# Optimization experiments

Measured on AMD Instinct MI355X. Metric: run time of the kernel, lower is better.

Reference implementation:

```python
import jax, jax.numpy as jnp
import numpy as np

D = 384
MAXPOS = 6

def setup_inputs() -> dict:
    key = jax.random.key(0)
    ks = jax.random.split(key, 20)
    B, Lt, Lh, E = 4, 1024, 512, 64
    inp = {
        'text': jax.random.normal(ks[0], (B, Lt, D), jnp.float32),
        'html': jax.random.normal(ks[1], (B, Lh, D), jnp.float32),
        'H2Hmask': jax.random.randint(ks[2], (B, Lh, Lh), 0, E, jnp.int32),
        'T2Tmask': (jax.random.uniform(ks[3], (B, Lt, Lt)) < 0.1).astype(jnp.float32),
        'H2Tmask': (jax.random.uniform(ks[4], (B, Lh, Lt)) < 0.1).astype(jnp.float32),
        'T2Hmask': (jax.random.uniform(ks[5], (B, Lt, Lh)) < 0.1).astype(jnp.float32),
        'positionembedding': jax.random.normal(ks[6], (2 * MAXPOS + 1, D), jnp.float32) * 0.02,
        'htmledgeembedding': jax.random.normal(ks[7], (E, D), jnp.float32) * 0.02,
    }
    names = ['W_V_T', 'W_V_H', 'W_Q_H2H', 'W_K_H2H', 'W_Q_H2T', 'W_K_H2T',
             'W_Q_T2H', 'W_K_T2H', 'W_Q_T2T', 'W_K_T2T']
    lim = np.sqrt(6.0 / (D + D))  # glorot_uniform
    for i, n in enumerate(names):
        inp[n] = jax.random.uniform(ks[8 + i], (D, D), jnp.float32, -lim, lim)
    return inp


def _forward(text, html, H2Hmask, T2Tmask, H2Tmask, T2Hmask,
             positionembedding, htmledgeembedding,
             W_V_T, W_V_H, W_Q_H2H, W_K_H2H, W_Q_H2T, W_K_H2T,
             W_Q_T2H, W_K_T2H, W_Q_T2T, W_K_T2T):
    B, Lt, _ = text.shape
    Lh = html.shape[1]
    scale = 1.0 / jnp.sqrt(jnp.float32(D))

    text_v = text @ W_V_T   # (B,Lt,D)
    html_v = html @ W_V_H   # (B,Lh,D)

    # ---- H2H: content + gathered edge-embedding bias ----
    # sum_d q[b,i,d] * (k[b,j,d] + edge[H2Hmask[b,i,j], d])
    #   = (q k^T)[b,i,j] + (q E^T)[b,i, H2Hmask[b,i,j]]
    h2h_q = html @ W_Q_H2H
    h2h_k = html @ W_K_H2H
    h2h_content = jnp.einsum('bid,bjd->bij', h2h_q, h2h_k)
    qe = h2h_q @ htmledgeembedding.T                       # (B,Lh,E)
    h2h_bias = jnp.take_along_axis(qe, H2Hmask, axis=-1)   # (B,Lh,Lh)
    h2h_e = (h2h_content + h2h_bias) * scale
    h2h_e = h2h_e - 10000.0 * (H2Hmask == 0).astype(jnp.float32)
    html1 = jax.nn.softmax(h2h_e, axis=-1) @ html_v

    # ---- H2T ----
    h2t_e = jnp.einsum('bid,bjd->bij', html @ W_Q_H2T, text @ W_K_H2T) * scale
    h2t_e = h2t_e - 10000.0 * H2Tmask
    html2 = jax.nn.softmax(h2t_e, axis=-1) @ text_v

    # ---- T2H (note: original code never applies T2Hmask) ----
    t2h_e = jnp.einsum('bid,bjd->bij', text @ W_Q_T2H, html @ W_K_T2H) * scale
    text1 = jax.nn.softmax(t2h_e, axis=-1) @ html_v

    # ---- T2T: content + relative-position bias ----
    idx = jnp.arange(Lt, dtype=jnp.int32)
    pos_ids = jnp.clip(idx[None, :] - idx[:, None], -MAXPOS, MAXPOS) + MAXPOS  # (Lt,Lt)
    t2t_q = text @ W_Q_T2T
    t2t_k = text @ W_K_T2T
    t2t_content = jnp.einsum('bid,bjd->bij', t2t_q, t2t_k)
    qp = t2t_q @ positionembedding.T                       # (B,Lt,2*MAXPOS+1)
    t2t_bias = jnp.take_along_axis(
        qp, jnp.broadcast_to(pos_ids[None], (B, Lt, Lt)), axis=-1)
    t2t_e = (t2t_content + t2t_bias) * scale
    t2t_e = t2t_e - 10000.0 * T2Tmask
    text2 = jax.nn.softmax(t2t_e, axis=-1) @ text_v

    # concat updated text (Lt) and html (Lh) along seq axis -> (B, Lt+Lh, D)
    return jnp.concatenate([text1 + text2, html1 + html2], axis=1)


def reference(text, html, H2Hmask, T2Tmask, H2Tmask, T2Hmask,
              positionembedding, htmledgeembedding,
              W_V_T, W_V_H, W_Q_H2H, W_K_H2H, W_Q_H2T, W_K_H2T,
              W_Q_T2H, W_K_T2H, W_Q_T2T, W_K_T2T):
    return _forward(text, html, H2Hmask, T2Tmask, H2Tmask, T2Hmask,
                    positionembedding, htmledgeembedding,
                    W_V_T, W_V_H, W_Q_H2H, W_K_H2H, W_Q_H2T, W_K_H2T,
                    W_Q_T2H, W_K_T2H, W_Q_T2T, W_K_T2T)
```

## Files before the change

### kernel.cpp

```cpp
#include <hip/hip_runtime.h>
#include <math.h>

typedef unsigned short u16;
typedef unsigned int u32;
typedef __attribute__((ext_vector_type(8))) short short8;
typedef __attribute__((ext_vector_type(4))) float f32x4;

__device__ __forceinline__ u16 f2bf(float f) {
    u32 u = __float_as_uint(f);
    u = (u + 0x7FFFu + ((u >> 16) & 1u)) >> 16;
    return (u16)u;
}
__device__ __forceinline__ float bf2f(u16 h) {
    return __uint_as_float(((u32)h) << 16);
}


__global__ __launch_bounds__(256)
void cvt4(const float4* __restrict__ a, int na4,
          const float4* __restrict__ b, int nb4,
          const float4* __restrict__ c, int nc4,
          const float4* __restrict__ d, int nd4,
          u16* __restrict__ oa, u16* __restrict__ ob,
          u16* __restrict__ oc, u16* __restrict__ od)
{
    int idx = blockIdx.x * 256 + threadIdx.x;
    const int tot = na4 + nb4 + nc4 + nd4;
    for (; idx < tot; idx += gridDim.x * 256) {
        float4 v; u16* o;
        int t = idx;
        if (t < na4)      { v = a[t]; o = oa + (long)t * 4; }
        else if ((t -= na4) < nb4) { v = b[t]; o = ob + (long)t * 4; }
        else if ((t -= nb4) < nc4) { v = c[t]; o = oc + (long)t * 4; }
        else { t -= nc4;    v = d[t]; o = od + (long)t * 4; }
        u32 lo = (u32)f2bf(v.x) | ((u32)f2bf(v.y) << 16);
        u32 hi = (u32)f2bf(v.z) | ((u32)f2bf(v.w) << 16);
        uint2 pk; pk.x = lo; pk.y = hi;
        *reinterpret_cast<uint2*>(o) = pk;
    }
}

struct WP { const float* p[10]; };
struct WD { u16* d[10]; };

__global__ __launch_bounds__(1024)
void wtrans(WP w, WD wd)
{
    __shared__ float t[32][33];
    const int z = blockIdx.z;
    const float* W = w.p[z];
    const int k = blockIdx.x * 32 + threadIdx.y;
    const int n = blockIdx.y * 32 + threadIdx.x;
    t[threadIdx.y][threadIdx.x] = W[k * 384 + n];
    __syncthreads();
    const int no = blockIdx.y * 32 + threadIdx.y;
    const int ko = blockIdx.x * 32 + threadIdx.x;
    wd.d[z][no * 384 + ko] = f2bf(t[threadIdx.x][threadIdx.y]);
}

__device__ __forceinline__ void mfma_core128(
    const u16* __restrict__ A, int lda,
    const u16* __restrict__ B, int ldb, int K,
    u16* __restrict__ As, u16* __restrict__ Bs,
    f32x4 (&acc)[4][4])
{
    const int tid  = threadIdx.x;
    const int wid  = tid >> 6;
    const int lane = tid & 63;
    const int wr = wid >> 1, wc = wid & 1;
    const int lane15 = lane & 15;
    const int kg = (lane >> 4) * 8;
    const int srow = lane >> 2;
    const int scol = (lane & 3) * 8;

    #pragma unroll
    for (int i = 0; i < 4; ++i)
        #pragma unroll
        for (int j = 0; j < 4; ++j)
            acc[i][j] = (f32x4){0.f, 0.f, 0.f, 0.f};

    for (int k0 = 0; k0 < K; k0 += 32) {
        #pragma unroll
        for (int i = 0; i < 2; ++i) {
            const int rg = (wid * 2 + i) * 16;
            const u16* ga = A + (long)(rg + srow) * lda + (k0 + scol);
            const u16* gb = B + (long)(rg + srow) * ldb + (k0 + scol);
            u16* la = As + (wid * 2 + i) * 512;
            u16* lb = Bs + (wid * 2 + i) * 512;
            __builtin_amdgcn_global_load_lds(
                (const __attribute__((address_space(1))) void*)ga,
                (__attribute__((address_space(3))) void*)la, 16, 0, 0);
            __builtin_amdgcn_global_load_lds(
                (const __attribute__((address_space(1))) void*)gb,
                (__attribute__((address_space(3))) void*)lb, 16, 0, 0);
        }
        __syncthreads();

        short8 af[4], bf[4];
        #pragma unroll
        for (int mi = 0; mi < 4; ++mi)
            af[mi] = *reinterpret_cast<const short8*>(
                As + (wr * 64 + mi * 16 + lane15) * 32 + kg);
        #pragma unroll
        for (int ni = 0; ni < 4; ++ni)
            bf[ni] = *reinterpret_cast<const short8*>(
                Bs + (wc * 64 + ni * 16 + lane15) * 32 + kg);
        #pragma unroll
        for (int mi = 0; mi < 4; ++mi)
            #pragma unroll
            for (int ni = 0; ni < 4; ++ni)
                acc[mi][ni] = __builtin_amdgcn_mfma_f32_16x16x32_bf16(
                    af[mi], bf[ni], acc[mi][ni], 0, 0, 0);
        __syncthreads();
    }
}

struct Seg {
    const u16* A; const u16* B; float* C;
    long sA, sB, sC;
    int lda, ldb, ldc, K, nbx, nbxSh, start, pad;
};
struct Segs { Seg s[6]; };

template<int NSEG>
__global__ __launch_bounds__(256)
void gemm_grouped(Segs d)
{
    __shared__ __align__(16) u16 As[4096];
    __shared__ __align__(16) u16 Bs[4096];
    const int bid = blockIdx.x;
    Seg sg = d.s[0];
    if (NSEG > 1 && bid >= d.s[1].start) sg = d.s[1];
    if (NSEG > 2 && bid >= d.s[2].start) sg = d.s[2];
    if (NSEG > 3 && bid >= d.s[3].start) sg = d.s[3];
    if (NSEG > 4 && bid >= d.s[4].start) sg = d.s[4];
    if (NSEG > 5 && bid >= d.s[5].start) sg = d.s[5];

    const int local = bid - sg.start;
    const int bx = local & (sg.nbx - 1);
    const int by = local >> sg.nbxSh;
    const int z  = blockIdx.y;
    const int m0 = bx * 128, n0 = by * 128;

    const u16* A = sg.A + (long)z * sg.sA + (long)m0 * sg.lda;
    const u16* B = sg.B + (long)z * sg.sB + (long)n0 * sg.ldb;

    f32x4 acc[4][4];
    mfma_core128(A, sg.lda, B, sg.ldb, sg.K, As, Bs, acc);

    const int tid = threadIdx.x;
    const int wid = tid >> 6, lane = tid & 63;
    const int wr = wid >> 1, wc = wid & 1;
    const int lane15 = lane & 15;
    const int r0 = (lane >> 4) * 4;

    float* C = sg.C + (long)z * sg.sC;
    #pragma unroll
    for (int mi = 0; mi < 4; ++mi)
        #pragma unroll
        for (int r = 0; r < 4; ++r) {
            const int row = m0 + wr * 64 + mi * 16 + r0 + r;
            float* crow = C + (long)row * sg.ldc + n0 + wc * 64 + lane15;
            #pragma unroll
            for (int ni = 0; ni < 4; ++ni)
                crow[ni * 16] = acc[mi][ni][r];
        }
}

struct PSeg {
    const u16* A; const u16* Bw; u16* QK; u16* VT;
    int lvtSh, vtOff, nbx, nbxSh, start, pad;
};
struct PSegs { PSeg s[2]; };

__global__ __launch_bounds__(256)
void proj_grouped(PSegs d)
{
    __shared__ __align__(16) u16 As[4096];
    __shared__ __align__(16) u16 Bs[4096];
    const int bid = blockIdx.x;
    PSeg sg = d.s[0];
    if (bid >= d.s[1].start) sg = d.s[1];

    const int local = bid - sg.start;
    const int bx = local & (sg.nbx - 1);
    const int by = local >> sg.nbxSh;
    const int m0 = bx * 128, n0 = by * 128;

    const u16* A = sg.A + (long)m0 * 384;
    const u16* B = sg.Bw + (long)n0 * 384;

    f32x4 acc[4][4];
    mfma_core128(A, 384, B, 384, 384, As, Bs, acc);

    const int tid = threadIdx.x;
    const int wid = tid >> 6, lane = tid & 63;
    const int wr = wid >> 1, wc = wid & 1;
    const int lane15 = lane & 15;
    const int r0 = (lane >> 4) * 4;
    const int lmask = (1 << sg.lvtSh) - 1;

    if (n0 < 384) {
        #pragma unroll
        for (int mi = 0; mi < 4; ++mi) {
            const int row = m0 + wr * 64 + mi * 16 + r0;
            const int bz = row >> sg.lvtSh;
            const int l  = row & lmask;
            #pragma unroll
            for (int ni = 0; ni < 4; ++ni) {
                const int col = n0 + wc * 64 + ni * 16 + lane15;
                u32 lo = (u32)f2bf(acc[mi][ni][0]) | ((u32)f2bf(acc[mi][ni][1]) << 16);
                u32 hi = (u32)f2bf(acc[mi][ni][2]) | ((u32)f2bf(acc[mi][ni][3]) << 16);
                uint2 pk; pk.x = lo; pk.y = hi;
                *reinterpret_cast<uint2*>(
                    sg.VT + ((long)bz * 384 + col) * 1536 + sg.vtOff + l) = pk;
            }
        }
    } else {
        #pragma unroll
        for (int mi = 0; mi < 4; ++mi)
            #pragma unroll
            for (int r = 0; r < 4; ++r) {
                const int row = m0 + wr * 64 + mi * 16 + r0 + r;
                u16* qrow = sg.QK + (long)row * 1536 + (n0 - 384) + wc * 64 + lane15;
                #pragma unroll
                for (int ni = 0; ni < 4; ++ni)
                    qrow[ni * 16] = f2bf(acc[mi][ni][r]);
            }
    }
}


__device__ __forceinline__ float blockReduceMax(float v, float* red, int tid) {
    #pragma unroll
    for (int o = 32; o >= 1; o >>= 1) v = fmaxf(v, __shfl_xor(v, o));
    if ((tid & 63) == 0) red[tid >> 6] = v;
    __syncthreads();
    return fmaxf(fmaxf(red[0], red[1]), fmaxf(red[2], red[3]));
}
__device__ __forceinline__ float blockReduceSum(float v, float* red, int tid) {
    #pragma unroll
    for (int o = 32; o >= 1; o >>= 1) v += __shfl_xor(v, o);
    if ((tid & 63) == 0) red[4 + (tid >> 6)] = v;
    __syncthreads();
    return red[4] + red[5] + red[6] + red[7];
}

__global__ __launch_bounds__(256)
void softmax_fused(const float* __restrict__ scoresH, u16* __restrict__ probsH,
                   const float* __restrict__ scoresT, u16* __restrict__ probsT,
                   const float* __restrict__ qe, const float* __restrict__ qp,
                   const int* __restrict__ H2Hmask,
                   const float* __restrict__ H2Tmask,
                   const float* __restrict__ T2Tmask, float scale)
{
    const int bid = blockIdx.x;
    const int tid = threadIdx.x;
    __shared__ float qsh[64];
    __shared__ float red[8];

    if (bid < 2048) {
        const int b = bid >> 9, i = bid & 511;
        const long rbase = ((long)b * 512 + i) * 1536;
        const float* rowS = scoresH + rbase;
        u16* rowP = probsH + rbase;
        const int*   mrow  = H2Hmask + ((long)b * 512 + i) * 512;
        const float* m2row = H2Tmask + ((long)b * 512 + i) * 1024;
        if (tid < 64) qsh[tid] = qe[((long)b * 512 + i) * 128 + tid];
        __syncthreads();

        float x[2]; float mx = -1e30f;
        #pragma unroll
        for (int t = 0; t < 2; ++t) {
            const int j = tid + t * 256;
            const int m = mrow[j];
            float v = (rowS[j] + qsh[m]) * scale - 10000.f * (m == 0 ? 1.f : 0.f);
            x[t] = v; mx = fmaxf(mx, v);
        }
        mx = blockReduceMax(mx, red, tid);
        float s = 0.f;
        #pragma unroll
        for (int t = 0; t < 2; ++t) { x[t] = __expf(x[t] - mx); s += x[t]; }
        s = blockReduceSum(s, red, tid);
        float inv = 1.f / s;
        #pragma unroll
        for (int t = 0; t < 2; ++t) rowP[tid + t * 256] = f2bf(x[t] * inv);

        float y[4]; mx = -1e30f;
        #pragma unroll
        for (int t = 0; t < 4; ++t) {
            const int jj = tid + t * 256;
            float v = rowS[512 + jj] * scale - 10000.f * m2row[jj];
            y[t] = v; mx = fmaxf(mx, v);
        }
        mx = blockReduceMax(mx, red, tid);
        s = 0.f;
        #pragma unroll
        for (int t = 0; t < 4; ++t) { y[t] = __expf(y[t] - mx); s += y[t]; }
        s = blockReduceSum(s, red, tid);
        inv = 1.f / s;
        #pragma unroll
        for (int t = 0; t < 4; ++t) rowP[512 + tid + t * 256] = f2bf(y[t] * inv);
    } else {
        const int bid2 = bid - 2048;
        const int b = bid2 >> 10, i = bid2 & 1023;
        const long rbase = ((long)b * 1024 + i) * 1536;
        const float* rowS = scoresT + rbase;
        u16* rowP = probsT + rbase;
        const float* m2row = T2Tmask + ((long)b * 1024 + i) * 1024;
        if (tid < 13) qsh[tid] = qp[((long)b * 1024 + i) * 128 + tid];
        __syncthreads();

        float x[2]; float mx = -1e30f;
        #pragma unroll
        for (int t = 0; t < 2; ++t) {
            const int j = tid + t * 256;
            float v = rowS[j] * scale;
            x[t] = v; mx = fmaxf(mx, v);
        }
        mx = blockReduceMax(mx, red, tid);
        float s = 0.f;
        #pragma unroll
        for (int t = 0; t < 2; ++t) { x[t] = __expf(x[t] - mx); s += x[t]; }
        s = blockReduceSum(s, red, tid);
        float inv = 1.f / s;
        #pragma unroll
        for (int t = 0; t < 2; ++t) rowP[tid + t * 256] = f2bf(x[t] * inv);

        float y[4]; mx = -1e30f;
        #pragma unroll
        for (int t = 0; t < 4; ++t) {
            const int jj = tid + t * 256;
            int pos = jj - i;
            pos = (pos < -6 ? -6 : (pos > 6 ? 6 : pos)) + 6;
            float v = (rowS[512 + jj] + qsh[pos]) * scale - 10000.f * m2row[jj];
            y[t] = v; mx = fmaxf(mx, v);
        }
        mx = blockReduceMax(mx, red, tid);
        s = 0.f;
        #pragma unroll
        for (int t = 0; t < 4; ++t) { y[t] = __expf(y[t] - mx); s += y[t]; }
        s = blockReduceSum(s, red, tid);
        inv = 1.f / s;
        #pragma unroll
        for (int t = 0; t < 4; ++t) rowP[512 + tid + t * 256] = f2bf(y[t] * inv);
    }
}


extern "C" void kernel_launch(void* const* d_in, const int* in_sizes, int n_in,
                              void* d_out, int out_size, void* d_ws, size_t ws_size,
                              hipStream_t stream)
{
    const int Bn = 4, Lt = 1024, Lh = 512;
    const float scale = 0.05103103630798288f;

    const float* text    = (const float*)d_in[0];
    const float* html    = (const float*)d_in[1];
    const int*   H2Hmask = (const int*)  d_in[2];
    const float* T2Tmask = (const float*)d_in[3];
    const float* H2Tmask = (const float*)d_in[4];
    const float* posemb  = (const float*)d_in[6];
    const float* edgeemb = (const float*)d_in[7];
    float* out = (float*)d_out;

    char* p = (char*)d_ws;
    auto au16 = [&](long n) { u16* r = (u16*)p;  p += ((n * 2 + 255) & ~255L); return r; };
    auto af32 = [&](long n) { float* r = (float*)p; p += ((n * 4 + 255) & ~255L); return r; };

    const long nT = (long)Bn * Lt * 384;
    const long nH = (long)Bn * Lh * 384;
    u16* text_bf = au16(nT);
    u16* html_bf = au16(nH);
    u16* WTtext  = au16(5L * 384 * 384);
    u16* WThtml  = au16(5L * 384 * 384);
    u16* edge_bf = au16(128L * 384);
    u16* pos_bf  = au16(128L * 384);
    u16* textQK  = au16((long)Bn * Lt * 1536);
    u16* htmlQK  = au16((long)Bn * Lh * 1536);
    u16* VTs     = au16((long)Bn * 384 * 1536);
    float* qe = af32((long)Bn * Lh * 128);
    float* qp = af32((long)Bn * Lt * 128);
    float* scoresH = af32((long)Bn * Lh * 1536);
    float* scoresT = af32((long)Bn * Lt * 1536);
    u16* probsH = au16((long)Bn * Lh * 1536);
    u16* probsT = au16((long)Bn * Lt * 1536);

    cvt4<<<2048, 256, 0, stream>>>((const float4*)text, (int)(nT / 4),
                                   (const float4*)html, (int)(nH / 4),
                                   (const float4*)edgeemb, 64 * 384 / 4,
                                   (const float4*)posemb, 13 * 384 / 4,
                                   text_bf, html_bf, edge_bf, pos_bf);
    WP wp; WD wd;
    for (int i = 0; i < 10; ++i) wp.p[i] = (const float*)d_in[8 + i];
    const long WSZ = 147456;
    wd.d[0] = WTtext + 0 * WSZ;
    wd.d[1] = WThtml + 0 * WSZ;
    wd.d[2] = WThtml + 1 * WSZ;
    wd.d[3] = WThtml + 2 * WSZ;
    wd.d[4] = WThtml + 3 * WSZ;
    wd.d[5] = WTtext + 1 * WSZ;
    wd.d[6] = WTtext + 2 * WSZ;
    wd.d[7] = WThtml + 4 * WSZ;
    wd.d[8] = WTtext + 3 * WSZ;
    wd.d[9] = WTtext + 4 * WSZ;
    wtrans<<<dim3(12, 12, 10), dim3(32, 32), 0, stream>>>(wp, wd);

    u16* h2h_q = htmlQK + 0;     u16* h2h_k = htmlQK + 384;
    u16* h2t_q = htmlQK + 768;   u16* t2h_k = htmlQK + 1152;
    u16* h2t_k = textQK + 0;     u16* t2h_q = textQK + 384;
    u16* t2t_q = textQK + 768;   u16* t2t_k = textQK + 1152;

    PSegs pj;
    pj.s[0] = { text_bf, WTtext, textQK, VTs, 10, 512, 32, 5, 0,   0 };
    pj.s[1] = { html_bf, WThtml, htmlQK, VTs,  9,   0, 16, 4, 480, 0 };
    proj_grouped<<<720, 256, 0, stream>>>(pj);

    const long sQt = (long)Lt * 1536, sQh = (long)Lh * 1536;
    const long sSh = (long)Lh * 1536, sSt = (long)Lt * 1536;
    const long sV  = (long)384 * 1536;
    const long sOut = (long)(Lt + Lh) * 384;

    Segs sc;
    sc.s[0] = { h2h_q, h2h_k,  scoresH,       sQh, sQh, sSh, 1536, 1536, 1536, 384, 4, 2,   0, 0 };
    sc.s[1] = { h2t_q, h2t_k,  scoresH + 512, sQh, sQt, sSh, 1536, 1536, 1536, 384, 4, 2,  16, 0 };
    sc.s[2] = { t2h_q, t2h_k,  scoresT,       sQt, sQh, sSt, 1536, 1536, 1536, 384, 8, 3,  48, 0 };
    sc.s[3] = { t2t_q, t2t_k,  scoresT + 512, sQt, sQt, sSt, 1536, 1536, 1536, 384, 8, 3,  80, 0 };
    sc.s[4] = { h2h_q, edge_bf, qe,           sQh, 0,   (long)Lh * 128, 1536, 384, 128, 384, 4, 2, 144, 0 };
    sc.s[5] = { t2t_q, pos_bf,  qp,           sQt, 0,   (long)Lt * 128, 1536, 384, 128, 384, 8, 3, 148, 0 };
    gemm_grouped<6><<<dim3(156, 4), 256, 0, stream>>>(sc);

    softmax_fused<<<6144, 256, 0, stream>>>(scoresH, probsH, scoresT, probsT,
                                            qe, qp, H2Hmask, H2Tmask, T2Tmask,
                                            scale);

    Segs pv;
    pv.s[0] = { probsH, VTs, out + (long)Lt * 384, sQh, sV, sOut, 1536, 1536, 384, 1536, 4, 2,  0, 0 };
    pv.s[1] = { probsT, VTs, out,                  sQt, sV, sOut, 1536, 1536, 384, 1536, 8, 3, 12, 0 };
    pv.s[2] = pv.s[1]; pv.s[3] = pv.s[1]; pv.s[4] = pv.s[1]; pv.s[5] = pv.s[1];
    gemm_grouped<2><<<dim3(36, 4), 256, 0, stream>>>(pv);
}
```

Baseline: 209.6 us.

## Split-K the PV GEMM into four K chunks with atomic accumulation

The final probs×V GEMM, with K=1536, launched only 36×4 blocks. It is now split into four K slices of 384 each across 8 segments, giving 144×4 blocks. Partial results are combined with relaxed float atomic adds into an output zeroed by a memset. This targets low occupancy on the many-CU GPU, at the cost of an extra memset, atomic traffic, and non-deterministic summation order.

```diff
diff --git a/kernel.cpp b/kernel.cpp
--- a/kernel.cpp
+++ b/kernel.cpp
@@ -118,11 +118,11 @@
 struct Seg {
     const u16* A; const u16* B; float* C;
     long sA, sB, sC;
-    int lda, ldb, ldc, K, nbx, nbxSh, start, pad;
+    int lda, ldb, ldc, K, nbx, nbxSh, start, kOff;
 };
-struct Segs { Seg s[6]; };
-
-template<int NSEG>
+struct Segs { Seg s[8]; };
+
+template<int NSEG, bool ATOMIC>
 __global__ __launch_bounds__(256)
 void gemm_grouped(Segs d)
 {
@@ -135,6 +135,8 @@
     if (NSEG > 3 && bid >= d.s[3].start) sg = d.s[3];
     if (NSEG > 4 && bid >= d.s[4].start) sg = d.s[4];
     if (NSEG > 5 && bid >= d.s[5].start) sg = d.s[5];
+    if (NSEG > 6 && bid >= d.s[6].start) sg = d.s[6];
+    if (NSEG > 7 && bid >= d.s[7].start) sg = d.s[7];
 
     const int local = bid - sg.start;
     const int bx = local & (sg.nbx - 1);
@@ -142,8 +144,8 @@
     const int z  = blockIdx.y;
     const int m0 = bx * 128, n0 = by * 128;
 
-    const u16* A = sg.A + (long)z * sg.sA + (long)m0 * sg.lda;
-    const u16* B = sg.B + (long)z * sg.sB + (long)n0 * sg.ldb;
+    const u16* A = sg.A + (long)z * sg.sA + (long)m0 * sg.lda + sg.kOff;
+    const u16* B = sg.B + (long)z * sg.sB + (long)n0 * sg.ldb + sg.kOff;
 
     f32x4 acc[4][4];
     mfma_core128(A, sg.lda, B, sg.ldb, sg.K, As, Bs, acc);
@@ -162,8 +164,14 @@
             const int row = m0 + wr * 64 + mi * 16 + r0 + r;
             float* crow = C + (long)row * sg.ldc + n0 + wc * 64 + lane15;
             #pragma unroll
-            for (int ni = 0; ni < 4; ++ni)
-                crow[ni * 16] = acc[mi][ni][r];
+            for (int ni = 0; ni < 4; ++ni) {
+                if (ATOMIC)
+                    __hip_atomic_fetch_add(crow + ni * 16, acc[mi][ni][r],
+                                           __ATOMIC_RELAXED,
+                                           __HIP_MEMORY_SCOPE_AGENT);
+                else
+                    crow[ni * 16] = acc[mi][ni][r];
+            }
         }
 }
 
@@ -428,15 +436,23 @@
     sc.s[3] = { t2t_q, t2t_k,  scoresT + 512, sQt, sQt, sSt, 1536, 1536, 1536, 384, 8, 3,  80, 0 };
     sc.s[4] = { h2h_q, edge_bf, qe,           sQh, 0,   (long)Lh * 128, 1536, 384, 128, 384, 4, 2, 144, 0 };
     sc.s[5] = { t2t_q, pos_bf,  qp,           sQt, 0,   (long)Lt * 128, 1536, 384, 128, 384, 8, 3, 148, 0 };
-    gemm_grouped<6><<<dim3(156, 4), 256, 0, stream>>>(sc);
+    sc.s[6] = sc.s[5]; sc.s[7] = sc.s[5];
+    gemm_grouped<6, false><<<dim3(156, 4), 256, 0, stream>>>(sc);
 
     softmax_fused<<<6144, 256, 0, stream>>>(scoresH, probsH, scoresT, probsT,
                                             qe, qp, H2Hmask, H2Tmask, T2Tmask,
                                             scale);
 
+    hipMemsetAsync(out, 0, (size_t)out_size * sizeof(float), stream);
+    float* outH = out + (long)Lt * 384;
     Segs pv;
-    pv.s[0] = { probsH, VTs, out + (long)Lt * 384, sQh, sV, sOut, 1536, 1536, 384, 1536, 4, 2,  0, 0 };
-    pv.s[1] = { probsT, VTs, out,                  sQt, sV, sOut, 1536, 1536, 384, 1536, 8, 3, 12, 0 };
-    pv.s[2] = pv.s[1]; pv.s[3] = pv.s[1]; pv.s[4] = pv.s[1]; pv.s[5] = pv.s[1];
-    gemm_grouped<2><<<dim3(36, 4), 256, 0, stream>>>(pv);
-}
+    pv.s[0] = { probsH, VTs, outH, sQh, sV, sOut, 1536, 1536, 384, 384, 4, 2,   0, 0    };
+    pv.s[1] = { probsH, VTs, outH, sQh, sV, sOut, 1536, 1536, 384, 384, 4, 2,  12, 384  };
+    pv.s[2] = { probsH, VTs, outH, sQh, sV, sOut, 1536, 1536, 384, 384, 4, 2,  24, 768  };
+    pv.s[3] = { probsH, VTs, outH, sQh, sV, sOut, 1536, 1536, 384, 384, 4, 2,  36, 1152 };
+    pv.s[4] = { probsT, VTs, out,  sQt, sV, sOut, 1536, 1536, 384, 384, 8, 3,  48, 0    };
+    pv.s[5] = { probsT, VTs, out,  sQt, sV, sOut, 1536, 1536, 384, 384, 8, 3,  72, 384  };
+    pv.s[6] = { probsT, VTs, out,  sQt, sV, sOut, 1536, 1536, 384, 384, 8, 3,  96, 768  };
+    pv.s[7] = { probsT, VTs, out,  sQt, sV, sOut, 1536, 1536, 384, 384, 8, 3, 120, 1152 };
+    gemm_grouped<8, true><<<dim3(144, 4), 256, 0, stream>>>(pv);
+}
```

After: 217.7 us. +3.9%, slower.
